# Kernel tuning notes

Hardware: AMD Instinct MI355X
Metric: run time of the kernel (lower is better)

## Reference

```python
import jax, jax.numpy as jnp
import numpy as np

B, S, D = 2, 2048, 2048
H, HKV = 16, 4
HD = D // H  # 128
ROPE_BASE = 10000.0


def _rope(t, cos, sin):
    # t: [B, h, S, HD]; torch variant: x1 = even dims, x2 = odd dims,
    # output = concat([x1*cos - x2*sin, x1*sin + x2*cos], axis=-1)
    x1 = t[..., ::2]
    x2 = t[..., 1::2]
    return jnp.concatenate([x1 * cos - x2 * sin, x1 * sin + x2 * cos], axis=-1)


def setup_inputs() -> dict:
    key = jax.random.key(0)
    kx, kq, kk, kv, ko = jax.random.split(key, 5)
    x = jax.random.normal(kx, (B, S, D), dtype=jnp.float32)
    scale = 0.02
    Wq = jax.random.normal(kq, (D, H * HD), dtype=jnp.float32) * scale
    Wk = jax.random.normal(kk, (D, HKV * HD), dtype=jnp.float32) * scale
    Wv = jax.random.normal(kv, (D, HKV * HD), dtype=jnp.float32) * scale
    Wo = jax.random.normal(ko, (H * HD, D), dtype=jnp.float32) * scale
    mask = jnp.tril(jnp.ones((S, S), dtype=bool))  # causal
    return {"x": x, "Wq": Wq, "Wk": Wk, "Wv": Wv, "Wo": Wo, "mask": mask}


def reference(x, Wq, Wk, Wv, Wo, mask):
    b, s, d = x.shape
    # projections: [B,S,h,HD] -> [B,h,S,HD]
    q = (x @ Wq).reshape(b, s, H, HD).transpose(0, 2, 1, 3)
    k = (x @ Wk).reshape(b, s, HKV, HD).transpose(0, 2, 1, 3)
    v = (x @ Wv).reshape(b, s, HKV, HD).transpose(0, 2, 1, 3)

    # RoPE tables: [S, HD/2]
    theta = 1.0 / (ROPE_BASE ** (jnp.arange(0, HD, 2, dtype=jnp.float32) / HD))
    angles = jnp.arange(s, dtype=jnp.float32)[:, None] * theta
    cos, sin = jnp.cos(angles), jnp.sin(angles)

    q = _rope(q, cos, sin)
    k = _rope(k, cos, sin)

    # GQA: repeat_interleave kv heads along head dim
    rep = H // HKV
    k = jnp.repeat(k, rep, axis=1)
    v = jnp.repeat(v, rep, axis=1)

    scores = jnp.einsum("bhqd,bhkd->bhqk", q, k) / jnp.sqrt(jnp.float32(HD))
    scores = jnp.where(mask, scores, -jnp.inf)
    attn = jax.nn.softmax(scores, axis=-1)

    out = jnp.einsum("bhqk,bhkd->bqhd", attn, v).reshape(b, s, H * HD)
    return out @ Wo
```

## Files before the change

kernel.cpp:

```cpp
#include <hip/hip_runtime.h>

typedef __bf16 bf16;
typedef __bf16 bf16x8 __attribute__((ext_vector_type(8)));
typedef float f32x4 __attribute__((ext_vector_type(4)));
typedef short s16x4 __attribute__((ext_vector_type(4)));

#define B_ 2
#define S_ 2048
#define D_ 2048
#define H_ 16
#define HKV_ 4
#define HD_ 128
#define QKVW 3072
#define QKW 2560
#define SCALE 0.08838834764831845f
#define NEGINF -30000.0f

__device__ inline void gload16(const void* g, void* l) {
  __builtin_amdgcn_global_load_lds((const __attribute__((address_space(1))) unsigned int*)g,
                                   (__attribute__((address_space(3))) unsigned int*)l, 16, 0, 0);
}

__device__ inline unsigned short bfb(float v) {
  union { bf16 h; unsigned short u; } c;
  c.h = (bf16)v;
  return c.u;
}

__global__ void detect_dtype(const unsigned* __restrict__ xw, int* __restrict__ flag) {
  __shared__ int cnt;
  if (threadIdx.x == 0) cnt = 0;
  __syncthreads();
  unsigned w = xw[(size_t)threadIdx.x * 16384];
  unsigned low = w & 0xFFFFu;
  int e = (int)((low >> 7) & 0xFF);
  int vote = (low == 0u || (e >= 100 && e <= 140)) ? 1 : 0;
  atomicAdd(&cnt, vote);
  __syncthreads();
  if (threadIdx.x == 0) *flag = (cnt >= 128) ? 1 : 0;
}

__global__ __launch_bounds__(256) void transpose_qkvw(
    const void* __restrict__ Wq, const void* __restrict__ Wk, const void* __restrict__ Wv,
    bf16* __restrict__ wqkvT, const int* __restrict__ flag) {
  int z = blockIdx.z;
  const void* in = (z == 0) ? Wq : (z == 1) ? Wk : Wv;
  int cols = (z == 0) ? 2048 : 512;
  bf16* out = wqkvT + ((z == 0) ? 0 : (z == 1) ? 2048 * 2048 : 2560 * 2048);
  if (blockIdx.x * 32 >= cols) return;
  int fm = *flag;
  __shared__ float tile[32][33];
  int c0 = blockIdx.x * 32, r0 = blockIdx.y * 32;
  int tx = threadIdx.x, ty = threadIdx.y;
#pragma unroll
  for (int i = 0; i < 32; i += 8) {
    long idx = (long)(r0 + ty + i) * cols + c0 + tx;
    tile[ty + i][tx] = fm ? (float)((const bf16*)in)[idx] : ((const float*)in)[idx];
  }
  __syncthreads();
#pragma unroll
  for (int i = 0; i < 32; i += 8)
    out[(long)(c0 + ty + i) * 2048 + r0 + tx] = (bf16)tile[tx][ty + i];
}

__global__ __launch_bounds__(256) void transpose_cvt(
    const void* __restrict__ in, bf16* __restrict__ out,
    long in_stride, long out_stride, const int* __restrict__ flag) {
  __shared__ float tile[32][33];
  int fm = *flag;
  int c0 = blockIdx.x * 32, r0 = blockIdx.y * 32;
  int tx = threadIdx.x, ty = threadIdx.y;
#pragma unroll
  for (int i = 0; i < 32; i += 8) {
    long idx = (long)(r0 + ty + i) * in_stride + c0 + tx;
    tile[ty + i][tx] = fm ? (float)((const bf16*)in)[idx] : ((const float*)in)[idx];
  }
  __syncthreads();
#pragma unroll
  for (int i = 0; i < 32; i += 8)
    out[(long)(c0 + ty + i) * out_stride + r0 + tx] = (bf16)tile[tx][ty + i];
}

#define BM 128
#define BN 128
#define BK 32

__global__ __launch_bounds__(256) void gemm_bt(
    const void* __restrict__ A, const bf16* __restrict__ Bt, void* __restrict__ C,
    int M, int N, int K, int ldc, int ncmax,
    bf16* __restrict__ vt_out, int vcol0,
    const int* __restrict__ flag, int adyn, int cdyn) {
  alignas(16) __shared__ bf16 la[2 * BM * BK];
  alignas(16) __shared__ bf16 lb[2 * BN * BK];
  int fm = flag ? *flag : 1;
  bool af32 = adyn && !fm;
  bool cf32 = cdyn && !fm;
  int tid = threadIdx.x;
  int wave = tid >> 6, lane = tid & 63;
  int wr = wave >> 1, wc = wave & 1;
  int quad = lane >> 4, l16 = lane & 15;

  int nwg = (int)(gridDim.x * gridDim.y);
  int flat = (int)(blockIdx.y * gridDim.x + blockIdx.x);
  int cpx = nwg >> 3;
  int wk = (flat & 7) * cpx + (flat >> 3);
  int bx = wk % (int)gridDim.x, by = wk / (int)gridDim.x;
  int m0 = by * BM, n0 = bx * BN;

  f32x4 acc[4][4] = {};

  int sr = (wave << 4) + (lane >> 2);
  int sc = (lane & 3) << 3;
  const bf16* gb0 = Bt + (long)(n0 + sr) * K + sc;
  const bf16* gb1 = Bt + (long)(n0 + 64 + sr) * K + sc;
  int lo0 = (wave << 9);
  int lo1 = 2048 + (wave << 9);
  const bf16* ga0 = nullptr; const bf16* ga1 = nullptr;
  const float* gaf = nullptr;
  int fr = tid >> 1, fh = (tid & 1) << 4;
  if (af32) gaf = (const float*)A + (long)(m0 + fr) * K + fh;
  else { ga0 = (const bf16*)A + (long)(m0 + sr) * K + sc;
         ga1 = (const bf16*)A + (long)(m0 + 64 + sr) * K + sc; }
  int lawo = fr * BK + fh;

  int nk = K / BK;

  gload16(gb0, lb + lo0);
  gload16(gb1, lb + lo1);
  if (af32) {
    float4 f0[4];
#pragma unroll
    for (int u = 0; u < 4; u++) f0[u] = *(const float4*)(gaf + 4 * u);
    alignas(16) bf16 tt[16];
#pragma unroll
    for (int u = 0; u < 4; u++) {
      tt[4 * u] = (bf16)f0[u].x; tt[4 * u + 1] = (bf16)f0[u].y;
      tt[4 * u + 2] = (bf16)f0[u].z; tt[4 * u + 3] = (bf16)f0[u].w;
    }
    *(uint4*)(la + lawo) = *(uint4*)tt;
    *(uint4*)(la + lawo + 8) = *(uint4*)(tt + 8);
  } else {
    gload16(ga0, la + lo0);
    gload16(ga1, la + lo1);
  }
  __syncthreads();

  for (int t = 0; t < nk; ++t) {
    int cur = t & 1, nxt = cur ^ 1;
    const bf16* laC = la + (cur << 12);
    const bf16* lbC = lb + (cur << 12);
    bool hasnext = (t + 1 < nk);
    float4 f[4];
    if (hasnext) {
      int k0 = (t + 1) * BK;
      gload16(gb0 + k0, lb + (nxt << 12) + lo0);
      gload16(gb1 + k0, lb + (nxt << 12) + lo1);
      if (af32) {
        const float* fp = gaf + k0;
#pragma unroll
        for (int u = 0; u < 4; u++) f[u] = *(const float4*)(fp + 4 * u);
      } else {
        gload16(ga0 + k0, la + (nxt << 12) + lo0);
        gload16(ga1 + k0, la + (nxt << 12) + lo1);
      }
    }

    const bf16* pa = laC + ((wr << 6) + l16) * BK + (quad << 3);
    const bf16* pb = lbC + ((wc << 6) + l16) * BK + (quad << 3);
    bf16x8 af[4], bfr[4];
#pragma unroll
    for (int i = 0; i < 4; i++) af[i] = *(const bf16x8*)(pa + (i << 4) * BK);
#pragma unroll
    for (int j = 0; j < 4; j++) bfr[j] = *(const bf16x8*)(pb + (j << 4) * BK);
#pragma unroll
    for (int i = 0; i < 4; i++)
#pragma unroll
      for (int j = 0; j < 4; j++)
        acc[i][j] = __builtin_amdgcn_mfma_f32_16x16x32_bf16(af[i], bfr[j], acc[i][j], 0, 0, 0);

    if (hasnext && af32) {
      alignas(16) bf16 tt[16];
#pragma unroll
      for (int u = 0; u < 4; u++) {
        tt[4 * u] = (bf16)f[u].x; tt[4 * u + 1] = (bf16)f[u].y;
        tt[4 * u + 2] = (bf16)f[u].z; tt[4 * u + 3] = (bf16)f[u].w;
      }
      *(uint4*)(la + (nxt << 12) + lawo) = *(uint4*)tt;
      *(uint4*)(la + (nxt << 12) + lawo + 8) = *(uint4*)(tt + 8);
    }
    __syncthreads();
  }

  if (vt_out && n0 >= vcol0) {
#pragma unroll
    for (int i = 0; i < 4; i++)
#pragma unroll
      for (int j = 0; j < 4; j++) {
        int col = n0 + (wc << 6) + (j << 4) + l16;
        int hdg = col - vcol0;
        int row0 = m0 + (wr << 6) + (i << 4) + (quad << 2);
        int bb = row0 >> 11, s = row0 & 2047;
        ushort4 p;
        p.x = bfb(acc[i][j][0]); p.y = bfb(acc[i][j][1]);
        p.z = bfb(acc[i][j][2]); p.w = bfb(acc[i][j][3]);
        *(ushort4*)(vt_out + (((long)(bb * 512 + hdg)) << 11) + s) = p;
      }
  } else {
#pragma unroll
    for (int i = 0; i < 4; i++)
#pragma unroll
      for (int j = 0; j < 4; j++) {
        int col = n0 + (wc << 6) + (j << 4) + l16;
        if (col >= ncmax) continue;
#pragma unroll
        for (int r = 0; r < 4; r++) {
          long row = m0 + (wr << 6) + (i << 4) + (quad << 2) + r;
          float v = acc[i][j][r];
          if (cf32) ((float*)C)[row * ldc + col] = v;
          else      ((bf16*)C)[row * ldc + col] = (bf16)v;
        }
      }
  }
}

__global__ __launch_bounds__(256) void rope_scatter(
    const bf16* __restrict__ qkv, bf16* __restrict__ Q, bf16* __restrict__ Ko) {
  int row = blockIdx.x;
  int b = row >> 11, s = row & 2047;
  int tid = threadIdx.x;
  const bf16* src = qkv + (long)row * QKW;
#pragma unroll
  for (int it = 0; it < 4; ++it) {
    int p = tid + it * 256;
    int h = p >> 6, i = p & 63;
    float x1 = (float)src[h * 128 + 2 * i];
    float x2 = (float)src[h * 128 + 2 * i + 1];
    float theta = __expf(-0.14391156831212787f * (float)i);
    float sn, cs;
    sincosf((float)s * theta, &sn, &cs);
    long qb = ((long)(b * H_ + h) * S_ + s) * HD_;
    Q[qb + i]      = (bf16)((x1 * cs - x2 * sn) * SCALE);
    Q[qb + 64 + i] = (bf16)((x1 * sn + x2 * cs) * SCALE);
  }
  {
    int kh = tid >> 6, i = tid & 63;
    float x1 = (float)src[2048 + kh * 128 + 2 * i];
    float x2 = (float)src[2048 + kh * 128 + 2 * i + 1];
    float theta = __expf(-0.14391156831212787f * (float)i);
    float sn, cs;
    sincosf((float)s * theta, &sn, &cs);
    long kb = ((long)(b * HKV_ + kh) * S_ + s) * HD_;
    Ko[kb + i]      = (bf16)(x1 * cs - x2 * sn);
    Ko[kb + 64 + i] = (bf16)(x1 * sn + x2 * cs);
  }
}

#define KTILE 8192
#define VTILE 8192

__global__ __launch_bounds__(256) void attn_kernel(
    const bf16* __restrict__ Q, const bf16* __restrict__ K,
    const bf16* __restrict__ Vt, bf16* __restrict__ O) {
  alignas(16) __shared__ bf16 Ks[2 * KTILE];
  alignas(16) __shared__ bf16 Vs[2 * VTILE];
  int qt0 = blockIdx.x;
  int h = blockIdx.y, b = blockIdx.z;
  int kh = h >> 2;
  int tid = threadIdx.x, wave = tid >> 6, lane = tid & 63;
  int quad = lane >> 4, l16 = lane & 15;
  const bf16* Kg = K + ((long)(b * HKV_ + kh) * S_) * HD_;
  const bf16* Vg = Vt + ((long)(b * HKV_ + kh) * HD_) * S_;

  int kgo[4], vgo[4], klo[4], vlo[4];
#pragma unroll
  for (int u = 0; u < 4; u++) {
    int i = u * 4 + wave;
    int r = i * 4 + quad;
    int c = l16 ^ (r & 15);
    kgo[u] = r * HD_ + c * 8;
    klo[u] = i * 512;
    int v = i * 8 + (lane >> 3);
    int cv = (lane & 7) ^ (v & 7);
    vgo[u] = v * S_ + cv * 8;
    vlo[u] = i * 512;
  }

  for (int hf = 0; hf < 2; ++hf) {
    int qt = hf ? 31 - qt0 : qt0;
    int q0 = qt * 64;
    const bf16* Qg = Q + ((long)(b * H_ + h) * S_ + q0) * HD_;

    bf16x8 qb[4];
    {
      const bf16* qrow = Qg + (wave * 16 + l16) * HD_ + quad * 8;
#pragma unroll
      for (int kk = 0; kk < 4; kk++) qb[kk] = *(const bf16x8*)(qrow + kk * 32);
    }

    if (hf) __syncthreads();

#pragma unroll
    for (int u = 0; u < 4; u++) {
      gload16(Kg + kgo[u], Ks + klo[u]);
      gload16(Vg + vgo[u], Vs + vlo[u]);
    }

    f32x4 Of[8] = {};
    float m_run = NEGINF, l_run = 0.f;

    for (int kt = 0; kt <= qt; ++kt) {
      __syncthreads();
      int p = kt & 1;
      if (kt < qt) {
        const bf16* kn = Kg + (long)(kt + 1) * 8192;
        const bf16* vn = Vg + (long)(kt + 1) * 64;
        bf16* kd = Ks + (p ^ 1) * KTILE;
        bf16* vd = Vs + (p ^ 1) * VTILE;
#pragma unroll
        for (int u = 0; u < 4; u++) {
          gload16(kn + kgo[u], kd + klo[u]);
          gload16(vn + vgo[u], vd + vlo[u]);
        }
      }
      const bf16* kc = Ks + p * KTILE;
      const bf16* vc = Vs + p * VTILE;

      bool diag = (kt == qt);
      f32x4 sf[4];
      __builtin_amdgcn_s_setprio(1);
#pragma unroll
      for (int jb = 0; jb < 4; jb++) {
        if (diag && jb > wave) {
          sf[jb] = (f32x4){NEGINF, NEGINF, NEGINF, NEGINF};
        } else {
          f32x4 a = {};
          const bf16* kbase = kc + (jb * 16 + l16) * 128;
#pragma unroll
          for (int kk = 0; kk < 4; kk++) {
            bf16x8 kf = *(const bf16x8*)(kbase + (((kk * 4 + quad) ^ l16) * 8));
            a = __builtin_amdgcn_mfma_f32_16x16x32_bf16(kf, qb[kk], a, 0, 0, 0);
          }
          sf[jb] = a;
        }
      }
      __builtin_amdgcn_s_setprio(0);
      if (diag) {
#pragma unroll
        for (int jb = 0; jb < 4; jb++)
          if (jb == wave) {
#pragma unroll
            for (int r = 0; r < 4; r++)
              if (quad * 4 + r > l16) sf[jb][r] = NEGINF;
          }
      }

      float mx = NEGINF;
#pragma unroll
      for (int jb = 0; jb < 4; jb++)
#pragma unroll
        for (int r = 0; r < 4; r++) mx = fmaxf(mx, sf[jb][r]);
      mx = fmaxf(mx, __shfl_xor(mx, 16));
      mx = fmaxf(mx, __shfl_xor(mx, 32));
      if (__any(mx > m_run + 8.0f)) {
        float mnew = fmaxf(m_run, mx);
        float alpha = __expf(m_run - mnew);
        m_run = mnew;
        l_run *= alpha;
#pragma unroll
        for (int n = 0; n < 8; n++) Of[n] *= alpha;
      }

      float ls = 0.f;
      s16x4 pk[4];
#pragma unroll
      for (int jb = 0; jb < 4; jb++) {
        float p0 = __expf(sf[jb][0] - m_run);
        float p1 = __expf(sf[jb][1] - m_run);
        float p2 = __expf(sf[jb][2] - m_run);
        float p3 = __expf(sf[jb][3] - m_run);
        ls += (p0 + p1) + (p2 + p3);
        s16x4 t;
        t.x = (short)bfb(p0); t.y = (short)bfb(p1);
        t.z = (short)bfb(p2); t.w = (short)bfb(p3);
        pk[jb] = t;
      }
      l_run += ls;

      __builtin_amdgcn_s_setprio(1);
#pragma unroll
      for (int jb = 0; jb < 4; jb++) {
        if (diag && jb > wave) continue;
#pragma unroll
        for (int n = 0; n < 8; n++) {
          int v = n * 16 + l16;
          const bf16* va_p = vc + v * 64 + (((jb * 2 + (quad >> 1)) ^ (l16 & 7)) * 8) + (quad & 1) * 4;
          s16x4 va = *(const s16x4*)va_p;
          Of[n] = __builtin_amdgcn_mfma_f32_16x16x16bf16_1k(va, pk[jb], Of[n], 0, 0, 0);
        }
      }
      __builtin_amdgcn_s_setprio(0);
    }

    l_run += __shfl_xor(l_run, 16);
    l_run += __shfl_xor(l_run, 32);
    float inv = 1.0f / fmaxf(l_run, 1e-30f);
    bf16* Ob = O + ((long)(b * S_) + q0 + wave * 16 + l16) * D_ + h * HD_;
#pragma unroll
    for (int n = 0; n < 8; n++) {
      ushort4 w;
      w.x = bfb(Of[n][0] * inv); w.y = bfb(Of[n][1] * inv);
      w.z = bfb(Of[n][2] * inv); w.w = bfb(Of[n][3] * inv);
      *(ushort4*)(Ob + n * 16 + quad * 4) = w;
    }
  }
}

extern "C" void kernel_launch(void* const* d_in, const int* in_sizes, int n_in,
                              void* d_out, int out_size, void* d_ws, size_t ws_size,
                              hipStream_t stream) {
  const void* x  = d_in[0];
  const void* Wq = d_in[1];
  const void* Wk = d_in[2];
  const void* Wv = d_in[3];
  const void* Wo = d_in[4];
  bf16* ws = (bf16*)d_ws;
  int* flag = (int*)d_ws;

  bf16* qkv   = ws + 16;
  bf16* Vtb   = ws + 10485776;
  bf16* Qb    = ws + 12582928;
  bf16* wqkvT = ws + 12582928;
  bf16* Kb    = ws + 20971536;
  bf16* attno = ws + 16;
  bf16* woT   = ws + 10485776;

  dim3 tb(32, 8);
  detect_dtype<<<1, 256, 0, stream>>>((const unsigned*)x, flag);
  transpose_qkvw<<<dim3(64, 64, 3), tb, 0, stream>>>(Wq, Wk, Wv, wqkvT, flag);
  gemm_bt<<<dim3(QKVW / BN, (B_ * S_) / BM), 256, 0, stream>>>(
      x, wqkvT, qkv, B_ * S_, QKVW, D_, QKW, QKW, Vtb, QKW, flag, 1, 0);
  rope_scatter<<<B_ * S_, 256, 0, stream>>>(qkv, Qb, Kb);
  attn_kernel<<<dim3(S_ / 128, H_, B_), 256, 0, stream>>>(Qb, Kb, Vtb, attno);
  transpose_cvt<<<dim3(64, 64, 1), tb, 0, stream>>>(Wo, woT, 2048, 2048, flag);
  gemm_bt<<<dim3(D_ / BN, (B_ * S_) / BM), 256, 0, stream>>>(
      attno, woT, d_out, B_ * S_, D_, D_, D_, D_, nullptr, 0, flag, 0, 1);
}
```

Baseline: 383.3 us.

## Triple-buffer GEMM LDS staging with explicit waitcnt-based pipelining

Moves the projection GEMM's shared-memory staging from two buffers to three, so global-to-LDS loads run two k-tiles ahead of the MFMA compute. The generic __syncthreads loop is replaced with raw s_barrier plus explicit vmcnt/lgkmcnt waits, which let loads for later tiles stay in flight during compute. The fp32-A path keeps its register prefetch and bf16 conversion, now spread across iterations. The change raises LDS use per block, which could reduce occupancy. The hand-counted waitcnt values must match the exact number of issued loads, so any mismatch would silently cause data races.

```diff
diff --git a/kernel.cpp b/kernel.cpp
--- a/kernel.cpp
+++ b/kernel.cpp
@@ -90,8 +90,8 @@
     int M, int N, int K, int ldc, int ncmax,
     bf16* __restrict__ vt_out, int vcol0,
     const int* __restrict__ flag, int adyn, int cdyn) {
-  alignas(16) __shared__ bf16 la[2 * BM * BK];
-  alignas(16) __shared__ bf16 lb[2 * BN * BK];
+  alignas(16) __shared__ bf16 la[3 * BM * BK];
+  alignas(16) __shared__ bf16 lb[3 * BN * BK];
   int fm = flag ? *flag : 1;
   bool af32 = adyn && !fm;
   bool cf32 = cdyn && !fm;
@@ -125,70 +125,88 @@
 
   int nk = K / BK;
 
-  gload16(gb0, lb + lo0);
-  gload16(gb1, lb + lo1);
-  if (af32) {
-    float4 f0[4];
-#pragma unroll
-    for (int u = 0; u < 4; u++) f0[u] = *(const float4*)(gaf + 4 * u);
+  auto stageB = [&](int T, int buf) {
+    int k0 = T * BK;
+    bf16* d = lb + (buf << 12);
+    gload16(gb0 + k0, d + lo0);
+    gload16(gb1 + k0, d + lo1);
+  };
+  auto stageA = [&](int T, int buf) {
+    int k0 = T * BK;
+    bf16* d = la + (buf << 12);
+    gload16(ga0 + k0, d + lo0);
+    gload16(ga1 + k0, d + lo1);
+  };
+  auto loadA = [&](int T, float4* f) {
+    const float* fp = gaf + (long)T * BK;
+#pragma unroll
+    for (int u = 0; u < 4; u++) f[u] = *(const float4*)(fp + 4 * u);
+  };
+  auto cvtwrite = [&](const float4* f, int buf) {
     alignas(16) bf16 tt[16];
 #pragma unroll
     for (int u = 0; u < 4; u++) {
-      tt[4 * u] = (bf16)f0[u].x; tt[4 * u + 1] = (bf16)f0[u].y;
-      tt[4 * u + 2] = (bf16)f0[u].z; tt[4 * u + 3] = (bf16)f0[u].w;
-    }
-    *(uint4*)(la + lawo) = *(uint4*)tt;
-    *(uint4*)(la + lawo + 8) = *(uint4*)(tt + 8);
+      tt[4 * u] = (bf16)f[u].x; tt[4 * u + 1] = (bf16)f[u].y;
+      tt[4 * u + 2] = (bf16)f[u].z; tt[4 * u + 3] = (bf16)f[u].w;
+    }
+    bf16* d = la + (buf << 12) + lawo;
+    *(uint4*)d = *(uint4*)tt;
+    *(uint4*)(d + 8) = *(uint4*)(tt + 8);
+  };
+  auto compute = [&](int buf) {
+    const bf16* pa = la + (buf << 12) + ((wr << 6) + l16) * BK + (quad << 3);
+    const bf16* pb = lb + (buf << 12) + ((wc << 6) + l16) * BK + (quad << 3);
+    bf16x8 afr[4], bfr[4];
+#pragma unroll
+    for (int i = 0; i < 4; i++) afr[i] = *(const bf16x8*)(pa + (i << 4) * BK);
+#pragma unroll
+    for (int j = 0; j < 4; j++) bfr[j] = *(const bf16x8*)(pb + (j << 4) * BK);
+#pragma unroll
+    for (int i = 0; i < 4; i++)
+#pragma unroll
+      for (int j = 0; j < 4; j++)
+        acc[i][j] = __builtin_amdgcn_mfma_f32_16x16x32_bf16(afr[i], bfr[j], acc[i][j], 0, 0, 0);
+  };
+
+  if (!af32) {
+    stageB(0, 0); stageA(0, 0);
+    stageB(1, 1); stageA(1, 1);
+    for (int t = 0; t + 2 < nk; ++t) {
+      int bS = (t + 2) % 3, bC = t % 3;
+      stageB(t + 2, bS);
+      stageA(t + 2, bS);
+      asm volatile("s_waitcnt vmcnt(8)" ::: "memory");
+      __builtin_amdgcn_s_barrier();
+      compute(bC);
+      __builtin_amdgcn_s_barrier();
+    }
+    asm volatile("s_waitcnt vmcnt(4)" ::: "memory");
+    __builtin_amdgcn_s_barrier();
+    compute((nk - 2) % 3);
+    asm volatile("s_waitcnt vmcnt(0)" ::: "memory");
+    __builtin_amdgcn_s_barrier();
+    compute((nk - 1) % 3);
   } else {
-    gload16(ga0, la + lo0);
-    gload16(ga1, la + lo1);
-  }
-  __syncthreads();
-
-  for (int t = 0; t < nk; ++t) {
-    int cur = t & 1, nxt = cur ^ 1;
-    const bf16* laC = la + (cur << 12);
-    const bf16* lbC = lb + (cur << 12);
-    bool hasnext = (t + 1 < nk);
-    float4 f[4];
-    if (hasnext) {
-      int k0 = (t + 1) * BK;
-      gload16(gb0 + k0, lb + (nxt << 12) + lo0);
-      gload16(gb1 + k0, lb + (nxt << 12) + lo1);
-      if (af32) {
-        const float* fp = gaf + k0;
-#pragma unroll
-        for (int u = 0; u < 4; u++) f[u] = *(const float4*)(fp + 4 * u);
-      } else {
-        gload16(ga0 + k0, la + (nxt << 12) + lo0);
-        gload16(ga1 + k0, la + (nxt << 12) + lo1);
-      }
-    }
-
-    const bf16* pa = laC + ((wr << 6) + l16) * BK + (quad << 3);
-    const bf16* pb = lbC + ((wc << 6) + l16) * BK + (quad << 3);
-    bf16x8 af[4], bfr[4];
-#pragma unroll
-    for (int i = 0; i < 4; i++) af[i] = *(const bf16x8*)(pa + (i << 4) * BK);
-#pragma unroll
-    for (int j = 0; j < 4; j++) bfr[j] = *(const bf16x8*)(pb + (j << 4) * BK);
-#pragma unroll
-    for (int i = 0; i < 4; i++)
-#pragma unroll
-      for (int j = 0; j < 4; j++)
-        acc[i][j] = __builtin_amdgcn_mfma_f32_16x16x32_bf16(af[i], bfr[j], acc[i][j], 0, 0, 0);
-
-    if (hasnext && af32) {
-      alignas(16) bf16 tt[16];
-#pragma unroll
-      for (int u = 0; u < 4; u++) {
-        tt[4 * u] = (bf16)f[u].x; tt[4 * u + 1] = (bf16)f[u].y;
-        tt[4 * u + 2] = (bf16)f[u].z; tt[4 * u + 3] = (bf16)f[u].w;
-      }
-      *(uint4*)(la + (nxt << 12) + lawo) = *(uint4*)tt;
-      *(uint4*)(la + (nxt << 12) + lawo + 8) = *(uint4*)(tt + 8);
-    }
-    __syncthreads();
+    float4 fP[4], fN[4];
+    stageB(0, 0); loadA(0, fP); cvtwrite(fP, 0);
+    stageB(1, 1); loadA(1, fP); cvtwrite(fP, 1);
+    for (int t = 0; t + 2 < nk; ++t) {
+      int bS = (t + 2) % 3, bC = t % 3;
+      stageB(t + 2, bS);
+      loadA(t + 2, fN);
+      if (t > 0) cvtwrite(fP, (t + 1) % 3);
+      asm volatile("s_waitcnt vmcnt(12) lgkmcnt(0)" ::: "memory");
+      __builtin_amdgcn_s_barrier();
+      compute(bC);
+      __builtin_amdgcn_s_barrier();
+#pragma unroll
+      for (int u = 0; u < 4; u++) fP[u] = fN[u];
+    }
+    cvtwrite(fP, (nk - 1) % 3);
+    compute((nk - 2) % 3);
+    asm volatile("s_waitcnt vmcnt(0) lgkmcnt(0)" ::: "memory");
+    __builtin_amdgcn_s_barrier();
+    compute((nk - 1) % 3);
   }
 
   if (vt_out && n0 >= vcol0) {
```

Result: slower. 440.1 us (+14.8%).

## Double GEMM K-tile to 64 with XOR-swizzled LDS layout

Applied to the files above, without the earlier changes.

Raises the GEMM K-tile from 32 to 64, which halves the number of barriers and main-loop iterations per output tile. It also replaces the linear LDS layout with an XOR-swizzled chunk layout so the 128-byte row stride does not cause bank conflicts on the fragment reads. The bf16 and fp32-A paths become separate loops so the common path carries no per-iteration branch. LDS use doubles to 64 KB per block, which may reduce occupancy.

```diff
diff --git a/kernel.cpp b/kernel.cpp
--- a/kernel.cpp
+++ b/kernel.cpp
@@ -83,7 +83,7 @@
 
 #define BM 128
 #define BN 128
-#define BK 32
+#define BK 64
 
 __global__ __launch_bounds__(256) void gemm_bt(
     const void* __restrict__ A, const bf16* __restrict__ Bt, void* __restrict__ C,
@@ -109,86 +109,106 @@
 
   f32x4 acc[4][4] = {};
 
-  int sr = (wave << 4) + (lane >> 2);
-  int sc = (lane & 3) << 3;
-  const bf16* gb0 = Bt + (long)(n0 + sr) * K + sc;
-  const bf16* gb1 = Bt + (long)(n0 + 64 + sr) * K + sc;
-  int lo0 = (wave << 9);
-  int lo1 = 2048 + (wave << 9);
-  const bf16* ga0 = nullptr; const bf16* ga1 = nullptr;
+  int drow = lane >> 3;
+  int dchunk = ((lane & 7) ^ drow) << 3;
+  long gbo[4], gao[4];
+  int ldsb[4];
+#pragma unroll
+  for (int u = 0; u < 4; u++) {
+    int rb = (wave << 5) + (u << 3);
+    int sr = rb + drow;
+    gbo[u] = (long)(n0 + sr) * K + dchunk;
+    gao[u] = (long)(m0 + sr) * K + dchunk;
+    ldsb[u] = rb << 6;
+  }
   const float* gaf = nullptr;
-  int fr = tid >> 1, fh = (tid & 1) << 4;
+  int fr = tid >> 1, fh = (tid & 1) << 5;
   if (af32) gaf = (const float*)A + (long)(m0 + fr) * K + fh;
-  else { ga0 = (const bf16*)A + (long)(m0 + sr) * K + sc;
-         ga1 = (const bf16*)A + (long)(m0 + 64 + sr) * K + sc; }
-  int lawo = fr * BK + fh;
 
   int nk = K / BK;
 
-  gload16(gb0, lb + lo0);
-  gload16(gb1, lb + lo1);
+  auto stageB = [&](int k0, bf16* dst) {
+#pragma unroll
+    for (int u = 0; u < 4; u++) gload16(Bt + gbo[u] + k0, dst + ldsb[u]);
+  };
+  auto stageA = [&](int k0, bf16* dst) {
+    const bf16* Ab = (const bf16*)A;
+#pragma unroll
+    for (int u = 0; u < 4; u++) gload16(Ab + gao[u] + k0, dst + ldsb[u]);
+  };
+  auto loadA = [&](int k0, float4* f) {
+    const float* fp = gaf + k0;
+#pragma unroll
+    for (int u = 0; u < 8; u++) f[u] = *(const float4*)(fp + 4 * u);
+  };
+  auto cvtwrite = [&](const float4* f, bf16* dbuf) {
+    int g = fr & 7, h4 = (tid & 1) << 2;
+    bf16* row = dbuf + (fr << 6);
+#pragma unroll
+    for (int cc = 0; cc < 4; cc++) {
+      alignas(16) bf16 tt[8];
+      float4 a = f[2 * cc], b2 = f[2 * cc + 1];
+      tt[0] = (bf16)a.x;  tt[1] = (bf16)a.y;  tt[2] = (bf16)a.z;  tt[3] = (bf16)a.w;
+      tt[4] = (bf16)b2.x; tt[5] = (bf16)b2.y; tt[6] = (bf16)b2.z; tt[7] = (bf16)b2.w;
+      *(uint4*)(row + (((h4 + cc) ^ g) << 3)) = *(uint4*)tt;
+    }
+  };
+  auto compute = [&](int buf) {
+    const bf16* pa = la + (buf << 13) + l16 * 64;
+    const bf16* pb = lb + (buf << 13) + l16 * 64;
+    int s7 = l16 & 7;
+#pragma unroll
+    for (int kk = 0; kk < 2; kk++) {
+      int co = (((kk << 2) + quad) ^ s7) << 3;
+      bf16x8 afr[4], bfr[4];
+#pragma unroll
+      for (int i = 0; i < 4; i++)
+        afr[i] = *(const bf16x8*)(pa + (((wr << 6) + (i << 4)) << 6) + co);
+#pragma unroll
+      for (int j = 0; j < 4; j++)
+        bfr[j] = *(const bf16x8*)(pb + (((wc << 6) + (j << 4)) << 6) + co);
+#pragma unroll
+      for (int i = 0; i < 4; i++)
+#pragma unroll
+        for (int j = 0; j < 4; j++)
+          acc[i][j] = __builtin_amdgcn_mfma_f32_16x16x32_bf16(afr[i], bfr[j], acc[i][j], 0, 0, 0);
+    }
+  };
+
+  stageB(0, lb);
   if (af32) {
-    float4 f0[4];
-#pragma unroll
-    for (int u = 0; u < 4; u++) f0[u] = *(const float4*)(gaf + 4 * u);
-    alignas(16) bf16 tt[16];
-#pragma unroll
-    for (int u = 0; u < 4; u++) {
-      tt[4 * u] = (bf16)f0[u].x; tt[4 * u + 1] = (bf16)f0[u].y;
-      tt[4 * u + 2] = (bf16)f0[u].z; tt[4 * u + 3] = (bf16)f0[u].w;
-    }
-    *(uint4*)(la + lawo) = *(uint4*)tt;
-    *(uint4*)(la + lawo + 8) = *(uint4*)(tt + 8);
+    float4 f0[8];
+    loadA(0, f0);
+    cvtwrite(f0, la);
   } else {
-    gload16(ga0, la + lo0);
-    gload16(ga1, la + lo1);
+    stageA(0, la);
   }
   __syncthreads();
 
-  for (int t = 0; t < nk; ++t) {
-    int cur = t & 1, nxt = cur ^ 1;
-    const bf16* laC = la + (cur << 12);
-    const bf16* lbC = lb + (cur << 12);
-    bool hasnext = (t + 1 < nk);
-    float4 f[4];
-    if (hasnext) {
-      int k0 = (t + 1) * BK;
-      gload16(gb0 + k0, lb + (nxt << 12) + lo0);
-      gload16(gb1 + k0, lb + (nxt << 12) + lo1);
-      if (af32) {
-        const float* fp = gaf + k0;
-#pragma unroll
-        for (int u = 0; u < 4; u++) f[u] = *(const float4*)(fp + 4 * u);
-      } else {
-        gload16(ga0 + k0, la + (nxt << 12) + lo0);
-        gload16(ga1 + k0, la + (nxt << 12) + lo1);
-      }
-    }
-
-    const bf16* pa = laC + ((wr << 6) + l16) * BK + (quad << 3);
-    const bf16* pb = lbC + ((wc << 6) + l16) * BK + (quad << 3);
-    bf16x8 af[4], bfr[4];
-#pragma unroll
-    for (int i = 0; i < 4; i++) af[i] = *(const bf16x8*)(pa + (i << 4) * BK);
-#pragma unroll
-    for (int j = 0; j < 4; j++) bfr[j] = *(const bf16x8*)(pb + (j << 4) * BK);
-#pragma unroll
-    for (int i = 0; i < 4; i++)
-#pragma unroll
-      for (int j = 0; j < 4; j++)
-        acc[i][j] = __builtin_amdgcn_mfma_f32_16x16x32_bf16(af[i], bfr[j], acc[i][j], 0, 0, 0);
-
-    if (hasnext && af32) {
-      alignas(16) bf16 tt[16];
-#pragma unroll
-      for (int u = 0; u < 4; u++) {
-        tt[4 * u] = (bf16)f[u].x; tt[4 * u + 1] = (bf16)f[u].y;
-        tt[4 * u + 2] = (bf16)f[u].z; tt[4 * u + 3] = (bf16)f[u].w;
-      }
-      *(uint4*)(la + (nxt << 12) + lawo) = *(uint4*)tt;
-      *(uint4*)(la + (nxt << 12) + lawo + 8) = *(uint4*)(tt + 8);
-    }
-    __syncthreads();
+  if (!af32) {
+    for (int t = 0; t < nk; ++t) {
+      int cur = t & 1, nxt = cur ^ 1;
+      if (t + 1 < nk) {
+        int k0 = (t + 1) * BK;
+        stageB(k0, lb + (nxt << 13));
+        stageA(k0, la + (nxt << 13));
+      }
+      compute(cur);
+      __syncthreads();
+    }
+  } else {
+    for (int t = 0; t < nk; ++t) {
+      int cur = t & 1, nxt = cur ^ 1;
+      float4 f[8];
+      if (t + 1 < nk) {
+        int k0 = (t + 1) * BK;
+        stageB(k0, lb + (nxt << 13));
+        loadA(k0, f);
+      }
+      compute(cur);
+      if (t + 1 < nk) cvtwrite(f, la + (nxt << 13));
+      __syncthreads();
+    }
   }
 
   if (vt_out && n0 >= vcol0) {
```

Measured after the change: 433.0 us. 1.13x slower.
